# Performance work log

Measured on AMD Instinct MI355X. Metric: run time of the kernel, lower is better.

Reference implementation:

```python
import jax, jax.numpy as jnp
import numpy as np

B, S, D, H = 4, 2048, 768, 12
DH = D // H  # 64


def setup_inputs() -> dict:
    key = jax.random.key(0)
    ks = jax.random.split(key, 7)
    return {
        "sequences": jax.random.normal(ks[0], (B, S, D), dtype=jnp.float32),
        "wq": jax.random.normal(ks[1], (H, DH, DH), dtype=jnp.float32) / np.sqrt(DH),
        "bq": jax.random.normal(ks[2], (H, DH), dtype=jnp.float32) * 0.02,
        "wk": jax.random.normal(ks[3], (H, DH, DH), dtype=jnp.float32) / np.sqrt(DH),
        "bk": jax.random.normal(ks[4], (H, DH), dtype=jnp.float32) * 0.02,
        "wv": jax.random.normal(ks[5], (H, DH, DH), dtype=jnp.float32) / np.sqrt(DH),
        "bv": jax.random.normal(ks[6], (H, DH), dtype=jnp.float32) * 0.02,
    }


def reference(sequences, wq, bq, wk, bk, wv, bv):
    # split channels into heads: [B, S, H, DH]
    xh = sequences.reshape(B, S, H, DH)
    # per-head linear projections (weight applied as x @ W^T + b, matching nn.Linear)
    q = jnp.einsum("bshd,hed->bshe", xh, wq) + bq  # [B,S,H,DH]
    k = jnp.einsum("bshd,hed->bshe", xh, wk) + bk
    v = jnp.einsum("bshd,hed->bshe", xh, wv) + bv
    scale = 1.0 / np.sqrt(DH).astype(np.float32)
    scores = jnp.einsum("bqhd,bkhd->bhqk", q, k) * scale  # [B,H,S,S]
    attn = jax.nn.softmax(scores, axis=-1)
    out = jnp.einsum("bhqk,bkhd->bqhd", attn, v)  # [B,S,H,DH]
    return out.reshape(B, S, D)
```

## Files before the change

kernel.cpp:

```cpp
#include <hip/hip_runtime.h>

#define NB 4
#define NS 2048
#define ND 768
#define NH 12
#define NDH 64
#define NT (NS / 128)
#define XPITCH 72
#define SSCALE 0.18033688011112043f

typedef __bf16 bf16x8 __attribute__((ext_vector_type(8)));
typedef float  f32x4  __attribute__((ext_vector_type(4)));
typedef unsigned int u32;

#define MFMA16(a, b, c) __builtin_amdgcn_mfma_f32_16x16x32_bf16(a, b, c, 0, 0, 0)

__device__ __forceinline__ u32 packbf(float a, float b) {
    u32 ua = __builtin_bit_cast(u32, a) + 0x8000u;
    u32 ub = __builtin_bit_cast(u32, b) + 0x8000u;
    return __builtin_amdgcn_perm(ub, ua, 0x07060302u);
}

__device__ __forceinline__ bf16x8 cvt8(float4 a, float4 b) {
    union { u32 u[4]; bf16x8 v; } r;
    r.u[0] = packbf(a.x, a.y); r.u[1] = packbf(a.z, a.w);
    r.u[2] = packbf(b.x, b.y); r.u[3] = packbf(b.z, b.w);
    return r.v;
}

__device__ __forceinline__ __bf16 f2bf(float f) {
    u32 u = __builtin_bit_cast(u32, f) + 0x8000u;
    unsigned short s = (unsigned short)(u >> 16);
    return __builtin_bit_cast(__bf16, s);
}

__global__ __launch_bounds__(256, 4) void proj_kernel(
    const float* __restrict__ x,
    const float* __restrict__ wq, const float* __restrict__ bq,
    const float* __restrict__ wk, const float* __restrict__ bk,
    const float* __restrict__ wv, const float* __restrict__ bv,
    __bf16* __restrict__ qws, __bf16* __restrict__ kws, __bf16* __restrict__ vtws)
{
    const int st = blockIdx.x, h = blockIdx.y, b = blockIdx.z;
    const int s0 = st * 64;
    const int tid = threadIdx.x;

    __shared__ __align__(16) __bf16 Xs[64 * XPITCH];
    __shared__ __align__(16) __bf16 Tv[64 * XPITCH];

    const int r = tid >> 2, f = tid & 3;
    const int lane = tid & 63, w = tid >> 6, col = lane & 15, quad = lane >> 4;

    const size_t wrow = (size_t)(h * NDH + w * 16 + col) * NDH;
    const float* wq0 = wq + wrow + quad * 8;
    const float* wk0 = wk + wrow + quad * 8;
    const float* wv0 = wv + wrow + quad * 8;
    const bf16x8 wqa0 = cvt8(*(const float4*)(wq0),      *(const float4*)(wq0 + 4));
    const bf16x8 wqa1 = cvt8(*(const float4*)(wq0 + 32), *(const float4*)(wq0 + 36));
    const bf16x8 wka0 = cvt8(*(const float4*)(wk0),      *(const float4*)(wk0 + 4));
    const bf16x8 wka1 = cvt8(*(const float4*)(wk0 + 32), *(const float4*)(wk0 + 36));
    const bf16x8 wva0 = cvt8(*(const float4*)(wv0),      *(const float4*)(wv0 + 4));
    const bf16x8 wva1 = cvt8(*(const float4*)(wv0 + 32), *(const float4*)(wv0 + 36));

    float bqs[4], bks[4], bvs[4];
#pragma unroll
    for (int rr = 0; rr < 4; ++rr) {
        const int e = h * NDH + w * 16 + quad * 4 + rr;
        bqs[rr] = bq[e] * SSCALE;
        bks[rr] = bk[e];
        bvs[rr] = bv[e];
    }

    const size_t bh = (size_t)(b * NH + h);

    {
        const float* xrow = x + (size_t)(b * NS + s0 + r) * ND + h * NDH + f * 16;
        const float4 v0 = *(const float4*)(xrow);
        const float4 v1 = *(const float4*)(xrow + 4);
        const float4 v2 = *(const float4*)(xrow + 8);
        const float4 v3 = *(const float4*)(xrow + 12);
        *(bf16x8*)&Xs[r * XPITCH + f * 16]     = cvt8(v0, v1);
        *(bf16x8*)&Xs[r * XPITCH + f * 16 + 8] = cvt8(v2, v3);
    }
    __syncthreads();

#pragma unroll
    for (int nt = 0; nt < 4; ++nt) {
        const bf16x8 xb0 = *(const bf16x8*)&Xs[(nt * 16 + col) * XPITCH + quad * 8];
        const bf16x8 xb1 = *(const bf16x8*)&Xs[(nt * 16 + col) * XPITCH + 32 + quad * 8];
        f32x4 aq = {0.f, 0.f, 0.f, 0.f};
        f32x4 ak = {0.f, 0.f, 0.f, 0.f};
        f32x4 av = {0.f, 0.f, 0.f, 0.f};
        aq = MFMA16(wqa0, xb0, aq); aq = MFMA16(wqa1, xb1, aq);
        ak = MFMA16(wka0, xb0, ak); ak = MFMA16(wka1, xb1, ak);
        av = MFMA16(wva0, xb0, av); av = MFMA16(wva1, xb1, av);

        union { u32 u[2]; uint2 v; } pq, pk;
        pq.u[0] = packbf(fmaf(aq[0], SSCALE, bqs[0]), fmaf(aq[1], SSCALE, bqs[1]));
        pq.u[1] = packbf(fmaf(aq[2], SSCALE, bqs[2]), fmaf(aq[3], SSCALE, bqs[3]));
        pk.u[0] = packbf(ak[0] + bks[0], ak[1] + bks[1]);
        pk.u[1] = packbf(ak[2] + bks[2], ak[3] + bks[3]);
        const size_t goff = (bh * NS + s0 + nt * 16 + col) * NDH + w * 16 + quad * 4;
        *(uint2*)(qws + goff) = pq.v;
        *(uint2*)(kws + goff) = pk.v;

        const int pos = ((nt >> 1) << 5) + ((col >> 2) << 3) + ((nt & 1) << 2) + (col & 3);
#pragma unroll
        for (int rr = 0; rr < 4; ++rr)
            Tv[(w * 16 + quad * 4 + rr) * XPITCH + pos] = f2bf(av[rr] + bvs[rr]);
    }
    __syncthreads();

    {
        const uint4 v0 = *(const uint4*)&Tv[r * XPITCH + f * 16];
        const uint4 v1 = *(const uint4*)&Tv[r * XPITCH + f * 16 + 8];
        __bf16* vdst = vtws + (bh * NDH + r) * NS + s0 + f * 16;
        *(uint4*)vdst = v0; *(uint4*)(vdst + 8) = v1;
    }
}

__global__ __launch_bounds__(256, 3) void attn_kernel(
    const __bf16* __restrict__ qws, const __bf16* __restrict__ kws,
    const __bf16* __restrict__ vtws, float* __restrict__ out)
{
    const int qt = blockIdx.x, h = blockIdx.y, b = blockIdx.z;
    const int q0 = qt * 64;
    const int tid = threadIdx.x;

    __shared__ __align__(16) unsigned char smem[36864];
    __bf16* lds = (__bf16*)smem;
    float* slabA = (float*)smem;
    float* slabB = (float*)(smem + 17408);
    float* lbuf  = (float*)(smem + 34816);

    const size_t bh = (size_t)(b * NH + h);
    const int lane = tid & 63, w = tid >> 6, col = lane & 15, quad = lane >> 4;
    const int L = lane;

    bf16x8 qb0[4], qb1[4];
#pragma unroll
    for (int nt = 0; nt < 4; ++nt) {
        const __bf16* qp = qws + (bh * NS + q0 + nt * 16 + col) * NDH + quad * 8;
        qb0[nt] = *(const bf16x8*)(qp);
        qb1[nt] = *(const bf16x8*)(qp + 32);
    }

    const __bf16* ksrc = kws + bh * (size_t)(NS * NDH)
                       + (size_t)(w * 32 + (L >> 3)) * NDH + ((L & 7) ^ (L >> 3)) * 8;
    const __bf16* vsrc = vtws + bh * (size_t)(NDH * NS)
                       + (size_t)(L >> 2) * NS + w * 32 + ((L & 3) ^ ((L >> 3) & 3)) * 8;
    const int kb_lds = w * 2048 + L * 8;
    const int vb_lds = 8192 + w * 2048 + L * 8;

    const int cx7 = col & 7;
    int ka_off[2][2], va_off[4];
#pragma unroll
    for (int mt = 0; mt < 2; ++mt) {
        const int base = w * 2048 + (mt * 16 + col) * 64;
        ka_off[mt][0] = base + ((quad)     ^ cx7) * 8;
        ka_off[mt][1] = base + ((quad + 4) ^ cx7) * 8;
    }
#pragma unroll
    for (int dt = 0; dt < 4; ++dt)
        va_off[dt] = 8192 + w * 2048 + (dt * 16 + col) * 32 + (quad ^ ((col >> 1) & 3)) * 8;

    float l[4] = {0.f, 0.f, 0.f, 0.f};
    f32x4 o[4][4];
#pragma unroll
    for (int dt = 0; dt < 4; ++dt)
#pragma unroll
        for (int nt = 0; nt < 4; ++nt) o[dt][nt] = (f32x4){0.f, 0.f, 0.f, 0.f};

    uint4 kstg[4], vstg[4];
#pragma unroll
    for (int i = 0; i < 4; ++i) kstg[i] = *(const uint4*)(ksrc + i * 512);
#pragma unroll
    for (int i = 0; i < 4; ++i) vstg[i] = *(const uint4*)(vsrc + (size_t)i * 16 * NS);
#pragma unroll
    for (int i = 0; i < 4; ++i) *(uint4*)&lds[kb_lds + i * 512] = kstg[i];
#pragma unroll
    for (int i = 0; i < 4; ++i) *(uint4*)&lds[vb_lds + i * 512] = vstg[i];

    for (int kt = 0; kt < NT; ++kt) {
        if (kt + 1 < NT) {
            const __bf16* ks = ksrc + (size_t)(kt + 1) * 8192;
            const __bf16* vs = vsrc + (kt + 1) * 128;
#pragma unroll
            for (int i = 0; i < 4; ++i) kstg[i] = *(const uint4*)(ks + i * 512);
#pragma unroll
            for (int i = 0; i < 4; ++i) vstg[i] = *(const uint4*)(vs + (size_t)i * 16 * NS);
        }

        bf16x8 ka[2][2], va[4];
#pragma unroll
        for (int mt = 0; mt < 2; ++mt) {
            ka[mt][0] = *(const bf16x8*)&lds[ka_off[mt][0]];
            ka[mt][1] = *(const bf16x8*)&lds[ka_off[mt][1]];
        }
#pragma unroll
        for (int dt = 0; dt < 4; ++dt) va[dt] = *(const bf16x8*)&lds[va_off[dt]];

#pragma unroll
        for (int nt = 0; nt < 4; ++nt) {
            f32x4 sA = {0.f, 0.f, 0.f, 0.f};
            f32x4 sB = {0.f, 0.f, 0.f, 0.f};
            sA = MFMA16(ka[0][0], qb0[nt], sA); sA = MFMA16(ka[0][1], qb1[nt], sA);
            sB = MFMA16(ka[1][0], qb0[nt], sB); sB = MFMA16(ka[1][1], qb1[nt], sB);

            const float p0 = __builtin_amdgcn_exp2f(sA[0]);
            const float p1 = __builtin_amdgcn_exp2f(sA[1]);
            const float p2 = __builtin_amdgcn_exp2f(sA[2]);
            const float p3 = __builtin_amdgcn_exp2f(sA[3]);
            const float p4 = __builtin_amdgcn_exp2f(sB[0]);
            const float p5 = __builtin_amdgcn_exp2f(sB[1]);
            const float p6 = __builtin_amdgcn_exp2f(sB[2]);
            const float p7 = __builtin_amdgcn_exp2f(sB[3]);
            l[nt] += ((p0 + p1) + (p2 + p3)) + ((p4 + p5) + (p6 + p7));

            union { u32 u[4]; bf16x8 v; } pb;
            pb.u[0] = packbf(p0, p1);
            pb.u[1] = packbf(p2, p3);
            pb.u[2] = packbf(p4, p5);
            pb.u[3] = packbf(p6, p7);

#pragma unroll
            for (int dt = 0; dt < 4; ++dt)
                o[dt][nt] = MFMA16(va[dt], pb.v, o[dt][nt]);
        }

        if (kt + 1 < NT) {
#pragma unroll
            for (int i = 0; i < 4; ++i) *(uint4*)&lds[kb_lds + i * 512] = kstg[i];
#pragma unroll
            for (int i = 0; i < 4; ++i) *(uint4*)&lds[vb_lds + i * 512] = vstg[i];
        }
    }

#pragma unroll
    for (int nt = 0; nt < 4; ++nt) {
        l[nt] += __shfl_xor(l[nt], 16, 64);
        l[nt] += __shfl_xor(l[nt], 32, 64);
    }

    __syncthreads();
    if (quad == 0) {
#pragma unroll
        for (int nt = 0; nt < 4; ++nt)
            lbuf[w * 64 + nt * 16 + col] = l[nt];
    }
    __syncthreads();

    float scale[4];
#pragma unroll
    for (int nt = 0; nt < 4; ++nt) {
        const int qi = nt * 16 + col;
        const float Lt = (lbuf[qi] + lbuf[64 + qi]) + (lbuf[128 + qi] + lbuf[192 + qi]);
        scale[nt] = 1.0f / Lt;
    }
    __syncthreads();
#pragma unroll
    for (int dt = 0; dt < 4; ++dt)
#pragma unroll
        for (int nt = 0; nt < 4; ++nt) o[dt][nt] *= scale[nt];

    if (w == 0 || w == 2) {
        float* s = (w == 0) ? slabA : slabB;
#pragma unroll
        for (int dt = 0; dt < 4; ++dt)
#pragma unroll
            for (int nt = 0; nt < 4; ++nt)
                *(f32x4*)&s[(nt * 16 + col) * 68 + dt * 16 + quad * 4] = o[dt][nt];
    }
    __syncthreads();
    if (w == 1 || w == 3) {
        float* s = (w == 1) ? slabA : slabB;
#pragma unroll
        for (int dt = 0; dt < 4; ++dt)
#pragma unroll
            for (int nt = 0; nt < 4; ++nt) {
                f32x4* p = (f32x4*)&s[(nt * 16 + col) * 68 + dt * 16 + quad * 4];
                *p = *p + o[dt][nt];
            }
    }
    __syncthreads();

    const int qr = tid >> 2, fq = tid & 3;
#pragma unroll
    for (int j = 0; j < 4; ++j) {
        const f32x4 a = *(const f32x4*)&slabA[qr * 68 + fq * 16 + j * 4];
        const f32x4 c = *(const f32x4*)&slabB[qr * 68 + fq * 16 + j * 4];
        *(f32x4*)&out[(size_t)(b * NS + q0 + qr) * ND + h * NDH + fq * 16 + j * 4] = a + c;
    }
}

extern "C" void kernel_launch(void* const* d_in, const int* in_sizes, int n_in,
                              void* d_out, int out_size, void* d_ws, size_t ws_size,
                              hipStream_t stream) {
    (void)in_sizes; (void)n_in; (void)out_size; (void)ws_size;
    const float* x  = (const float*)d_in[0];
    const float* wq = (const float*)d_in[1];
    const float* bq = (const float*)d_in[2];
    const float* wk = (const float*)d_in[3];
    const float* bk = (const float*)d_in[4];
    const float* wv = (const float*)d_in[5];
    const float* bv = (const float*)d_in[6];
    float* out = (float*)d_out;

    __bf16* qws  = (__bf16*)d_ws;
    __bf16* kws  = qws + (size_t)NB * NH * NS * NDH;
    __bf16* vtws = kws + (size_t)NB * NH * NS * NDH;

    dim3 grid(NS / 64, NH, NB);
    proj_kernel<<<grid, 256, 0, stream>>>(x, wq, bq, wk, bk, wv, bv, qws, kws, vtws);
    attn_kernel<<<grid, 256, 0, stream>>>(qws, kws, vtws, out);
}
```

Before: 176.3 us.

## Restructure projection to cover six heads per block, pre-convert weights, swizzle attention grid

Adds a small kernel that converts the projection weights to bf16 once per call. The projection kernel now loads a 32-row by 384-channel slab of x, making full-row reads more contiguous, and loops over six heads using the pre-converted bf16 weights. The V transpose goes through a small per-wave slab. The attention kernel uses a 1D grid remapped so that eight (batch, head) pairs are interleaved across consecutive blocks, which aims to improve K/V cache locality. This costs an extra kernel launch and some extra workspace.

```diff
diff --git a/kernel.cpp b/kernel.cpp
--- a/kernel.cpp
+++ b/kernel.cpp
@@ -6,7 +6,6 @@
 #define NH 12
 #define NDH 64
 #define NT (NS / 128)
-#define XPITCH 72
 #define SSCALE 0.18033688011112043f
 
 typedef __bf16 bf16x8 __attribute__((ext_vector_type(8)));
@@ -34,88 +33,100 @@
     return __builtin_bit_cast(__bf16, s);
 }
 
+__global__ __launch_bounds__(256) void wprep_kernel(
+    const float* __restrict__ wq, const float* __restrict__ wk,
+    const float* __restrict__ wv,
+    __bf16* __restrict__ wqb, __bf16* __restrict__ wkb, __bf16* __restrict__ wvb)
+{
+    const int i = (blockIdx.x * 256 + threadIdx.x) * 4;
+    float4 a;
+    uint2 p;
+    a = *(const float4*)(wq + i); p.x = packbf(a.x, a.y); p.y = packbf(a.z, a.w);
+    *(uint2*)(wqb + i) = p;
+    a = *(const float4*)(wk + i); p.x = packbf(a.x, a.y); p.y = packbf(a.z, a.w);
+    *(uint2*)(wkb + i) = p;
+    a = *(const float4*)(wv + i); p.x = packbf(a.x, a.y); p.y = packbf(a.z, a.w);
+    *(uint2*)(wvb + i) = p;
+}
+
 __global__ __launch_bounds__(256, 4) void proj_kernel(
     const float* __restrict__ x,
-    const float* __restrict__ wq, const float* __restrict__ bq,
-    const float* __restrict__ wk, const float* __restrict__ bk,
-    const float* __restrict__ wv, const float* __restrict__ bv,
+    const __bf16* __restrict__ wqb, const float* __restrict__ bq,
+    const __bf16* __restrict__ wkb, const float* __restrict__ bk,
+    const __bf16* __restrict__ wvb, const float* __restrict__ bv,
     __bf16* __restrict__ qws, __bf16* __restrict__ kws, __bf16* __restrict__ vtws)
 {
-    const int st = blockIdx.x, h = blockIdx.y, b = blockIdx.z;
-    const int s0 = st * 64;
+    const int st = blockIdx.x, hg = blockIdx.y, b = blockIdx.z;
+    const int s0 = st * 32;
     const int tid = threadIdx.x;
 
-    __shared__ __align__(16) __bf16 Xs[64 * XPITCH];
-    __shared__ __align__(16) __bf16 Tv[64 * XPITCH];
-
-    const int r = tid >> 2, f = tid & 3;
+    __shared__ __align__(16) __bf16 Xs[32 * 392];
+    __shared__ __align__(16) __bf16 Vslab[4][16 * 36];
+
     const int lane = tid & 63, w = tid >> 6, col = lane & 15, quad = lane >> 4;
 
-    const size_t wrow = (size_t)(h * NDH + w * 16 + col) * NDH;
-    const float* wq0 = wq + wrow + quad * 8;
-    const float* wk0 = wk + wrow + quad * 8;
-    const float* wv0 = wv + wrow + quad * 8;
-    const bf16x8 wqa0 = cvt8(*(const float4*)(wq0),      *(const float4*)(wq0 + 4));
-    const bf16x8 wqa1 = cvt8(*(const float4*)(wq0 + 32), *(const float4*)(wq0 + 36));
-    const bf16x8 wka0 = cvt8(*(const float4*)(wk0),      *(const float4*)(wk0 + 4));
-    const bf16x8 wka1 = cvt8(*(const float4*)(wk0 + 32), *(const float4*)(wk0 + 36));
-    const bf16x8 wva0 = cvt8(*(const float4*)(wv0),      *(const float4*)(wv0 + 4));
-    const bf16x8 wva1 = cvt8(*(const float4*)(wv0 + 32), *(const float4*)(wv0 + 36));
-
-    float bqs[4], bks[4], bvs[4];
-#pragma unroll
-    for (int rr = 0; rr < 4; ++rr) {
-        const int e = h * NDH + w * 16 + quad * 4 + rr;
-        bqs[rr] = bq[e] * SSCALE;
-        bks[rr] = bk[e];
-        bvs[rr] = bv[e];
-    }
-
-    const size_t bh = (size_t)(b * NH + h);
-
     {
-        const float* xrow = x + (size_t)(b * NS + s0 + r) * ND + h * NDH + f * 16;
-        const float4 v0 = *(const float4*)(xrow);
-        const float4 v1 = *(const float4*)(xrow + 4);
-        const float4 v2 = *(const float4*)(xrow + 8);
-        const float4 v3 = *(const float4*)(xrow + 12);
-        *(bf16x8*)&Xs[r * XPITCH + f * 16]     = cvt8(v0, v1);
-        *(bf16x8*)&Xs[r * XPITCH + f * 16 + 8] = cvt8(v2, v3);
-    }
-    __syncthreads();
-
-#pragma unroll
-    for (int nt = 0; nt < 4; ++nt) {
-        const bf16x8 xb0 = *(const bf16x8*)&Xs[(nt * 16 + col) * XPITCH + quad * 8];
-        const bf16x8 xb1 = *(const bf16x8*)&Xs[(nt * 16 + col) * XPITCH + 32 + quad * 8];
-        f32x4 aq = {0.f, 0.f, 0.f, 0.f};
-        f32x4 ak = {0.f, 0.f, 0.f, 0.f};
-        f32x4 av = {0.f, 0.f, 0.f, 0.f};
-        aq = MFMA16(wqa0, xb0, aq); aq = MFMA16(wqa1, xb1, aq);
-        ak = MFMA16(wka0, xb0, ak); ak = MFMA16(wka1, xb1, ak);
-        av = MFMA16(wva0, xb0, av); av = MFMA16(wva1, xb1, av);
-
-        union { u32 u[2]; uint2 v; } pq, pk;
-        pq.u[0] = packbf(fmaf(aq[0], SSCALE, bqs[0]), fmaf(aq[1], SSCALE, bqs[1]));
-        pq.u[1] = packbf(fmaf(aq[2], SSCALE, bqs[2]), fmaf(aq[3], SSCALE, bqs[3]));
-        pk.u[0] = packbf(ak[0] + bks[0], ak[1] + bks[1]);
-        pk.u[1] = packbf(ak[2] + bks[2], ak[3] + bks[3]);
-        const size_t goff = (bh * NS + s0 + nt * 16 + col) * NDH + w * 16 + quad * 4;
-        *(uint2*)(qws + goff) = pq.v;
-        *(uint2*)(kws + goff) = pk.v;
-
-        const int pos = ((nt >> 1) << 5) + ((col >> 2) << 3) + ((nt & 1) << 2) + (col & 3);
-#pragma unroll
-        for (int rr = 0; rr < 4; ++rr)
-            Tv[(w * 16 + quad * 4 + rr) * XPITCH + pos] = f2bf(av[rr] + bvs[rr]);
-    }
-    __syncthreads();
-
-    {
-        const uint4 v0 = *(const uint4*)&Tv[r * XPITCH + f * 16];
-        const uint4 v1 = *(const uint4*)&Tv[r * XPITCH + f * 16 + 8];
-        __bf16* vdst = vtws + (bh * NDH + r) * NS + s0 + f * 16;
-        *(uint4*)vdst = v0; *(uint4*)(vdst + 8) = v1;
+        const int row = tid >> 3, seg = tid & 7;
+        const float* xr = x + (size_t)(b * NS + s0 + row) * ND + hg * 384 + seg * 48;
+#pragma unroll
+        for (int j = 0; j < 6; ++j) {
+            const float4 f0 = *(const float4*)(xr + j * 8);
+            const float4 f1 = *(const float4*)(xr + j * 8 + 4);
+            *(bf16x8*)&Xs[row * 392 + seg * 48 + j * 8] = cvt8(f0, f1);
+        }
+    }
+    __syncthreads();
+
+    for (int hl = 0; hl < 6; ++hl) {
+        const int h = hg * 6 + hl;
+        const size_t bh = (size_t)(b * NH + h);
+
+        const size_t wr = ((size_t)(h * NDH + w * 16 + col)) * NDH + quad * 8;
+        const bf16x8 aq0 = *(const bf16x8*)(wqb + wr);
+        const bf16x8 aq1 = *(const bf16x8*)(wqb + wr + 32);
+        const bf16x8 ak0 = *(const bf16x8*)(wkb + wr);
+        const bf16x8 ak1 = *(const bf16x8*)(wkb + wr + 32);
+        const bf16x8 av0 = *(const bf16x8*)(wvb + wr);
+        const bf16x8 av1 = *(const bf16x8*)(wvb + wr + 32);
+
+        const float4 bqv = *(const float4*)(bq + h * NDH + w * 16 + quad * 4);
+        const float4 bkv = *(const float4*)(bk + h * NDH + w * 16 + quad * 4);
+        const float4 bvv = *(const float4*)(bv + h * NDH + w * 16 + quad * 4);
+        const float bqs[4] = {bqv.x * SSCALE, bqv.y * SSCALE, bqv.z * SSCALE, bqv.w * SSCALE};
+        const float bks[4] = {bkv.x, bkv.y, bkv.z, bkv.w};
+        const float bvs[4] = {bvv.x, bvv.y, bvv.z, bvv.w};
+
+#pragma unroll
+        for (int nt = 0; nt < 2; ++nt) {
+            const bf16x8 xb0 = *(const bf16x8*)&Xs[(nt * 16 + col) * 392 + hl * 64 + quad * 8];
+            const bf16x8 xb1 = *(const bf16x8*)&Xs[(nt * 16 + col) * 392 + hl * 64 + 32 + quad * 8];
+            f32x4 cq = {0.f, 0.f, 0.f, 0.f};
+            f32x4 ck = {0.f, 0.f, 0.f, 0.f};
+            f32x4 cv = {0.f, 0.f, 0.f, 0.f};
+            cq = MFMA16(aq0, xb0, cq); cq = MFMA16(aq1, xb1, cq);
+            ck = MFMA16(ak0, xb0, ck); ck = MFMA16(ak1, xb1, ck);
+            cv = MFMA16(av0, xb0, cv); cv = MFMA16(av1, xb1, cv);
+
+            union { u32 u[2]; uint2 v; } pq, pk;
+            pq.u[0] = packbf(fmaf(cq[0], SSCALE, bqs[0]), fmaf(cq[1], SSCALE, bqs[1]));
+            pq.u[1] = packbf(fmaf(cq[2], SSCALE, bqs[2]), fmaf(cq[3], SSCALE, bqs[3]));
+            pk.u[0] = packbf(ck[0] + bks[0], ck[1] + bks[1]);
+            pk.u[1] = packbf(ck[2] + bks[2], ck[3] + bks[3]);
+            const size_t goff = (bh * NS + s0 + nt * 16 + col) * NDH + w * 16 + quad * 4;
+            *(uint2*)(qws + goff) = pq.v;
+            *(uint2*)(kws + goff) = pk.v;
+
+            const int pos = (col >> 2) * 8 + nt * 4 + (col & 3);
+#pragma unroll
+            for (int rr = 0; rr < 4; ++rr)
+                Vslab[w][(quad * 4 + rr) * 36 + pos] = f2bf(cv[rr] + bvs[rr]);
+        }
+
+        {
+            const int row = lane >> 2, scol = (lane & 3) * 8;
+            const uint4 vv = *(const uint4*)&Vslab[w][row * 36 + scol];
+            *(uint4*)(vtws + (bh * NDH + w * 16 + row) * NS + s0 + scol) = vv;
+        }
     }
 }
 
@@ -123,7 +134,10 @@
     const __bf16* __restrict__ qws, const __bf16* __restrict__ kws,
     const __bf16* __restrict__ vtws, float* __restrict__ out)
 {
-    const int qt = blockIdx.x, h = blockIdx.y, b = blockIdx.z;
+    const int bid = blockIdx.x;
+    const int bh_i = (bid & 7) + 8 * (bid >> 8);
+    const int qt = (bid >> 3) & 31;
+    const int b = bh_i / NH, h = bh_i - b * NH;
     const int q0 = qt * 64;
     const int tid = threadIdx.x;
 
@@ -133,7 +147,7 @@
     float* slabB = (float*)(smem + 17408);
     float* lbuf  = (float*)(smem + 34816);
 
-    const size_t bh = (size_t)(b * NH + h);
+    const size_t bh = (size_t)bh_i;
     const int lane = tid & 63, w = tid >> 6, col = lane & 15, quad = lane >> 4;
     const int L = lane;
 
@@ -306,11 +320,16 @@
     const float* bv = (const float*)d_in[6];
     float* out = (float*)d_out;
 
+    const size_t TEN = (size_t)NB * NH * NS * NDH;
     __bf16* qws  = (__bf16*)d_ws;
-    __bf16* kws  = qws + (size_t)NB * NH * NS * NDH;
-    __bf16* vtws = kws + (size_t)NB * NH * NS * NDH;
-
-    dim3 grid(NS / 64, NH, NB);
-    proj_kernel<<<grid, 256, 0, stream>>>(x, wq, bq, wk, bk, wv, bv, qws, kws, vtws);
-    attn_kernel<<<grid, 256, 0, stream>>>(qws, kws, vtws, out);
-}
+    __bf16* kws  = qws + TEN;
+    __bf16* vtws = kws + TEN;
+    __bf16* wqb  = vtws + TEN;
+    __bf16* wkb  = wqb + (size_t)NH * NDH * NDH;
+    __bf16* wvb  = wkb + (size_t)NH * NDH * NDH;
+
+    wprep_kernel<<<48, 256, 0, stream>>>(wq, wk, wv, wqb, wkb, wvb);
+    dim3 pgrid(NS / 32, 2, NB);
+    proj_kernel<<<pgrid, 256, 0, stream>>>(x, wqb, bq, wkb, bk, wvb, bv, qws, kws, vtws);
+    attn_kernel<<<NB * NH * (NS / 64), 256, 0, stream>>>(qws, kws, vtws, out);
+}
```

Result: no change. 179.0 us (+1.6%).
